# Optimization experiments

Measured on AMD Instinct MI355X. Metric: run time of the kernel, lower is better.

Reference implementation:

```python
import jax, jax.numpy as jnp
import numpy as np

DIVISOR = 2.0
POOL = (2, 2, 2)  # (pd, ph, pw); stride == kernel, no padding


def setup_inputs() -> dict:
    key = jax.random.key(0)
    k1, k2 = jax.random.split(key)
    N, C, D, H, W = 16, 32, 32, 64, 64
    o = jax.random.normal(k1, (N, C, D, H, W), dtype=jnp.float32)
    bias = jax.random.normal(k2, (C, 1, 1, 1), dtype=jnp.float32)
    return {"o": o, "bias": bias}


def reference(o, bias):
    # o: [N, C, D, H, W]; bias: [C, 1, 1, 1]
    N, C, D, H, W = o.shape
    pd, ph, pw = POOL
    PD, PH, PW = D // pd, H // ph, W // pw

    x = o / DIVISOR
    # Non-overlapping 3D max pool (kernel == stride, padding 0) via reshape.
    x = x.reshape(N, C, PD, pd, PH, ph, PW, pw)
    x = x.max(axis=(3, 5, 7))            # [N, C, PD, PH, PW]
    # Global average pool over pooled spatial dims.
    x = x.mean(axis=(2, 3, 4))           # [N, C]
    # Add per-channel bias, then sum over channels.
    x = x + bias.reshape(1, C)           # [N, C]
    out = x.sum(axis=1).reshape(N, 1, 1, 1)
    return out
```

## Files before the change

kernel.cpp:

```cpp
#include <hip/hip_runtime.h>

#define N_  16
#define C_  32
#define D_  32
#define H_  64
#define W_  64
#define PD_ 16
#define PH_ 32
#define PWQ 16

constexpr int   ITEMS_PER_N  = C_ * PD_ * PH_ * PWQ;
constexpr int   BLOCKS_PER_N = 128;
constexpr int   THREADS      = 256;
constexpr float SCALE = 0.5f / (float)(PD_ * PH_ * 32);

__global__ __launch_bounds__(THREADS) void pool_sum_kernel(
    const float* __restrict__ o, const float* __restrict__ bias,
    float* __restrict__ out)
{
    const int n      = blockIdx.x / BLOCKS_PER_N;
    const int blkInN = blockIdx.x % BLOCKS_PER_N;
    const float* base_n = o + (size_t)n * (C_ * D_ * H_ * W_);

    float acc = 0.0f;
    const int stride = BLOCKS_PER_N * THREADS;
    int idx = blkInN * THREADS + threadIdx.x;

    #pragma unroll 4
    for (; idx < ITEMS_PER_N; idx += stride) {
        const int pwq = idx & 15;
        const int ph  = (idx >> 4) & 31;
        const int pd  = (idx >> 9) & 15;
        const int c   = idx >> 13;
        const float* p = base_n + (((size_t)c * D_ + 2 * pd) * H_ + 2 * ph) * W_ + 4 * pwq;
        const float4 r0 = *(const float4*)(p);
        const float4 r1 = *(const float4*)(p + W_);
        const float4 r2 = *(const float4*)(p + H_ * W_);
        const float4 r3 = *(const float4*)(p + H_ * W_ + W_);
        const float m0 = fmaxf(fmaxf(fmaxf(r0.x, r0.y), fmaxf(r1.x, r1.y)),
                               fmaxf(fmaxf(r2.x, r2.y), fmaxf(r3.x, r3.y)));
        const float m1 = fmaxf(fmaxf(fmaxf(r0.z, r0.w), fmaxf(r1.z, r1.w)),
                               fmaxf(fmaxf(r2.z, r2.w), fmaxf(r3.z, r3.w)));
        acc += m0 + m1;
    }

    #pragma unroll
    for (int off = 32; off > 0; off >>= 1) acc += __shfl_down(acc, off, 64);

    __shared__ float smem[THREADS / 64];
    const int wave = threadIdx.x >> 6;
    const int lane = threadIdx.x & 63;
    if (lane == 0) smem[wave] = acc;
    __syncthreads();

    if (threadIdx.x == 0) {
        float s = smem[0] + smem[1] + smem[2] + smem[3];
        s *= SCALE;
        if (blkInN == 0) {
            float bs = 0.0f;
            #pragma unroll
            for (int c = 0; c < C_; ++c) bs += bias[c];
            s += bs;
        }
        atomicAdd(&out[n], s);
    }
}

extern "C" void kernel_launch(void* const* d_in, const int* in_sizes, int n_in,
                              void* d_out, int out_size, void* d_ws, size_t ws_size,
                              hipStream_t stream) {
    const float* o    = (const float*)d_in[0];
    const float* bias = (const float*)d_in[1];
    float* out = (float*)d_out;

    hipMemsetAsync(out, 0, out_size * sizeof(float), stream);

    pool_sum_kernel<<<dim3(N_ * BLOCKS_PER_N), dim3(THREADS), 0, stream>>>(o, bias, out);
}
```

Measured before the change: 356.5 us.

## Replace memset and atomics with workspace partials and finalize kernel; unroll fixed loop

The strided grid loop becomes a fully unrolled loop of 8 iterations over channels with precomputed base addresses, so each thread issues more independent loads up front. Per-block partial sums now go to a workspace array, and a small second kernel reduces them and adds the bias. This removes the memset and the atomicAdd contention, at the cost of a second kernel launch. The outputs become deterministic, and the code assumes a workspace of at least 2048 floats.

```diff
diff --git a/kernel.cpp b/kernel.cpp
--- a/kernel.cpp
+++ b/kernel.cpp
@@ -5,38 +5,35 @@
 #define D_  32
 #define H_  64
 #define W_  64
-#define PD_ 16
-#define PH_ 32
-#define PWQ 16
 
-constexpr int   ITEMS_PER_N  = C_ * PD_ * PH_ * PWQ;
-constexpr int   BLOCKS_PER_N = 128;
-constexpr int   THREADS      = 256;
-constexpr float SCALE = 0.5f / (float)(PD_ * PH_ * 32);
+constexpr int BLOCKS_PER_N = 128;
+constexpr int THREADS      = 256;
+constexpr float SCALE = 0.5f / (float)(16 * 32 * 32);
 
-__global__ __launch_bounds__(THREADS) void pool_sum_kernel(
-    const float* __restrict__ o, const float* __restrict__ bias,
-    float* __restrict__ out)
+__global__ __launch_bounds__(THREADS) void pool_partial_kernel(
+    const float* __restrict__ o, float* __restrict__ ws)
 {
     const int n      = blockIdx.x / BLOCKS_PER_N;
     const int blkInN = blockIdx.x % BLOCKS_PER_N;
-    const float* base_n = o + (size_t)n * (C_ * D_ * H_ * W_);
+
+    const int t   = blkInN * THREADS + threadIdx.x;
+    const int pwq = t & 15;
+    const int ph  = (t >> 4) & 31;
+    const int pd  = (t >> 9) & 15;
+    const int c0  = t >> 13;
+
+    const float* p = o + (size_t)n * (C_ * D_ * H_ * W_)
+                       + (((size_t)c0 * D_ + 2 * pd) * H_ + 2 * ph) * W_ + 4 * pwq;
+    constexpr size_t CSTRIDE = (size_t)4 * D_ * H_ * W_;
 
     float acc = 0.0f;
-    const int stride = BLOCKS_PER_N * THREADS;
-    int idx = blkInN * THREADS + threadIdx.x;
-
-    #pragma unroll 4
-    for (; idx < ITEMS_PER_N; idx += stride) {
-        const int pwq = idx & 15;
-        const int ph  = (idx >> 4) & 31;
-        const int pd  = (idx >> 9) & 15;
-        const int c   = idx >> 13;
-        const float* p = base_n + (((size_t)c * D_ + 2 * pd) * H_ + 2 * ph) * W_ + 4 * pwq;
-        const float4 r0 = *(const float4*)(p);
-        const float4 r1 = *(const float4*)(p + W_);
-        const float4 r2 = *(const float4*)(p + H_ * W_);
-        const float4 r3 = *(const float4*)(p + H_ * W_ + W_);
+    #pragma unroll
+    for (int k = 0; k < 8; ++k) {
+        const float* q = p + k * CSTRIDE;
+        const float4 r0 = *(const float4*)(q);
+        const float4 r1 = *(const float4*)(q + W_);
+        const float4 r2 = *(const float4*)(q + H_ * W_);
+        const float4 r3 = *(const float4*)(q + H_ * W_ + W_);
         const float m0 = fmaxf(fmaxf(fmaxf(r0.x, r0.y), fmaxf(r1.x, r1.y)),
                                fmaxf(fmaxf(r2.x, r2.y), fmaxf(r3.x, r3.y)));
         const float m1 = fmaxf(fmaxf(fmaxf(r0.z, r0.w), fmaxf(r1.z, r1.w)),
@@ -48,22 +45,23 @@
     for (int off = 32; off > 0; off >>= 1) acc += __shfl_down(acc, off, 64);
 
     __shared__ float smem[THREADS / 64];
-    const int wave = threadIdx.x >> 6;
-    const int lane = threadIdx.x & 63;
-    if (lane == 0) smem[wave] = acc;
+    if ((threadIdx.x & 63) == 0) smem[threadIdx.x >> 6] = acc;
     __syncthreads();
+    if (threadIdx.x == 0)
+        ws[blockIdx.x] = smem[0] + smem[1] + smem[2] + smem[3];
+}
 
-    if (threadIdx.x == 0) {
-        float s = smem[0] + smem[1] + smem[2] + smem[3];
-        s *= SCALE;
-        if (blkInN == 0) {
-            float bs = 0.0f;
-            #pragma unroll
-            for (int c = 0; c < C_; ++c) bs += bias[c];
-            s += bs;
-        }
-        atomicAdd(&out[n], s);
-    }
+__global__ __launch_bounds__(64) void finalize_kernel(
+    const float* __restrict__ ws, const float* __restrict__ bias,
+    float* __restrict__ out)
+{
+    const int n    = blockIdx.x;
+    const int lane = threadIdx.x;
+    float acc = (ws[n * BLOCKS_PER_N + lane] + ws[n * BLOCKS_PER_N + 64 + lane]) * SCALE;
+    if (lane < C_) acc += bias[lane];
+    #pragma unroll
+    for (int off = 32; off > 0; off >>= 1) acc += __shfl_down(acc, off, 64);
+    if (lane == 0) out[n] = acc;
 }
 
 extern "C" void kernel_launch(void* const* d_in, const int* in_sizes, int n_in,
@@ -72,8 +70,8 @@
     const float* o    = (const float*)d_in[0];
     const float* bias = (const float*)d_in[1];
     float* out = (float*)d_out;
+    float* ws  = (float*)d_ws;
 
-    hipMemsetAsync(out, 0, out_size * sizeof(float), stream);
-
-    pool_sum_kernel<<<dim3(N_ * BLOCKS_PER_N), dim3(THREADS), 0, stream>>>(o, bias, out);
+    pool_partial_kernel<<<dim3(N_ * BLOCKS_PER_N), dim3(THREADS), 0, stream>>>(o, ws);
+    finalize_kernel<<<dim3(N_), dim3(64), 0, stream>>>(ws, bias, out);
 }
```

Result: no change. 355.2 us (-0.4%).
